# Performance work log

Measured on AMD Instinct MI355X. Metric: run time of the kernel, lower is better.

The kernel has to match this reference:

```python
import jax, jax.numpy as jnp
import numpy as np

MAXHD, MAXV, MINA, MAXA, DT = 100.0, 40.0, -4.0, 3.0, 0.1
NVEH, NT, H = 16384, 256, 20


def setup_inputs() -> dict:
    key = jax.random.key(0)
    ks = jax.random.split(key, 6)
    lead_speed = 10.0 + 5.0 * jax.random.normal(ks[0], (NVEH, NT), dtype=jnp.float32)
    lead_pos = 50.0 + 20.0 * jax.random.normal(ks[1], (NVEH, NT), dtype=jnp.float32)
    lead_inputs = jnp.stack([lead_pos, lead_speed], axis=2)  # (nveh, nt, 2)
    init_state = jnp.stack([
        5.0 * jax.random.normal(ks[2], (NVEH,), dtype=jnp.float32),
        10.0 + 2.0 * jax.random.normal(ks[3], (NVEH,), dtype=jnp.float32),
    ], axis=1)  # (nveh, 2) -> (pos, speed)
    return {
        "lead_inputs": lead_inputs,
        "init_state": init_state,
        "h0": jnp.zeros((NVEH, H), jnp.float32),
        "c0": jnp.zeros((NVEH, H), jnp.float32),
        "W": 0.3 * jax.random.normal(ks[4], (3, 4 * H), dtype=jnp.float32),
        "U": 0.2 * jax.random.normal(ks[5], (H, 4 * H), dtype=jnp.float32),
        "b": jnp.concatenate([jnp.zeros(H), jnp.ones(H), jnp.zeros(2 * H)]).astype(jnp.float32),  # unit forget bias
        "Wd": 0.3 * jax.random.normal(jax.random.fold_in(key, 7), (H, 1), dtype=jnp.float32),
        "bd": jnp.zeros((1,), jnp.float32),
    }


def reference(lead_inputs, init_state, h0, c0, W, U, b, Wd, bd):
    def step(carry, lead):
        pos, speed, h, c = carry
        curhd = (lead[:, 0] - pos) / MAXHD
        lead_v = lead[:, 1] / MAXV
        norm_v = speed / MAXV
        x = jnp.stack([curhd, norm_v, lead_v], axis=1)  # (nveh, 3)
        z = x @ W + h @ U + b  # (nveh, 4H), keras gate order i, f, g, o
        i, f, g, o = jnp.split(z, 4, axis=1)
        c = jax.nn.sigmoid(f) * c + jax.nn.sigmoid(i) * jnp.tanh(g)
        h = jax.nn.sigmoid(o) * jnp.tanh(c)
        out = (h @ Wd + bd)[:, 0]  # (nveh,)
        acc = (MAXA - MINA) * out + MINA
        speed = speed + DT * acc
        pos = pos + DT * acc  # faithful to source (uses acc, not speed)
        return (pos, speed, h, c), pos

    pos0, speed0 = init_state[:, 0], init_state[:, 1]
    (pos, speed, h, c), ys = jax.lax.scan(
        step, (pos0, speed0, h0, c0), jnp.swapaxes(lead_inputs, 0, 1))
    # tf.concat of nt (nveh,) tensors along -1 -> flat (nt*nveh,) in time-major order
    outputs = ys.reshape(-1)
    return outputs, speed, (h, c)
```

## Files before the change

### kernel.cpp

```cpp
#include <hip/hip_runtime.h>


#define NVEH 16384
#define NT   256
#define H    20

typedef float f32x4  __attribute__((ext_vector_type(4)));
typedef short bf16x8 __attribute__((ext_vector_type(8)));

#if __has_builtin(__builtin_amdgcn_exp2f)
#define EXP2(x) __builtin_amdgcn_exp2f(x)
#else
#define EXP2(x) __expf((x) * 0.69314718056f)
#endif
#define RCP(x) __builtin_amdgcn_rcpf(x)

__device__ __forceinline__ short f2bf(float f) {
    unsigned u = __builtin_bit_cast(unsigned, f);
    u += 0x7fffu + ((u >> 16) & 1u);
    return (short)(u >> 16);
}
__device__ __forceinline__ float bf2f(short s) {
    return __builtin_bit_cast(float, ((unsigned)(unsigned short)s) << 16);
}

__global__ __launch_bounds__(256, 1) void rnncf_kernel(
    const float* __restrict__ lead,
    const float* __restrict__ inits,
    const float* __restrict__ h0,
    const float* __restrict__ c0,
    const float* __restrict__ W,
    const float* __restrict__ U,
    const float* __restrict__ b,
    const float* __restrict__ Wd,
    const float* __restrict__ bd,
    float* __restrict__ out)
{
    __shared__ __attribute__((aligned(16))) short UT[96 * 32];

    const int tid  = threadIdx.x;
    const int lane = tid & 63;
    const int q    = lane >> 4;
    const int c    = lane & 15;
    const float L2E = 1.44269504f;
    const float N2L = -2.f * L2E;
    const float bdv = bd[0];
    const float biasK = 7.f * bdv - 4.f;

    for (int idx = tid; idx < 96 * 32; idx += 256) {
        int row = idx >> 5, k = idx & 31;
        int T = row >> 4, m = row & 15;
        int kq = k >> 3, ko = k & 7;
        float v = 0.f;
        if (T < 5) {
            int g = m & 3, j = 5 * (m >> 2) + T;
            int col = g * 20 + j;
            if      (ko < 5)             v = U[(5 * kq + ko) * 80 + col];
            else if (ko == 6 && kq < 3)  v = W[kq * 80 + col];
            else if (ko == 6)            v = b[col];
            v *= (g == 2) ? (2.f * L2E) : L2E;
        } else if ((m & 3) == 0) {
            if      (ko < 5)  v = 7.f * Wd[5 * kq + ko];
            else if (ko == 5) v = 1.f;
        }
        UT[idx] = f2bf(v);
    }

    const int veh = blockIdx.x * 64 + (tid >> 6) * 16 + c;

    float wcn[5][4], wd7[5], w7b[5];
#pragma unroll
    for (int T = 0; T < 5; ++T) {
        int j = 5 * q + T;
#pragma unroll
        for (int g = 0; g < 4; ++g) {
            int col = g * 20 + j;
            wcn[T][g] = -(-0.001f * W[col] + 0.0025f * W[80 + col])
                      * ((g == 2) ? (2.f * L2E) : L2E);
        }
        float w7 = 7.f * Wd[j];
        wd7[T] = w7;
        w7b[T] = bf2f(f2bf(w7));
    }

    bf16x8 Bf = {0, 0, 0, 0, 0, 0, 0, 0};
    float cst[5], hl[5];
    float rpart = 0.f, apart = 0.f;
#pragma unroll
    for (int T = 0; T < 5; ++T) {
        int j = 5 * q + T;
        float hv = h0[veh * H + j];
        cst[T] = c0[veh * H + j];
        hl[T] = hv;
        short hb = f2bf(hv);
        float hi = bf2f(hb);
        Bf[T] = hb;
        rpart = __builtin_fmaf(hv, wd7[T], rpart);
        rpart = __builtin_fmaf(-hi, w7b[T], rpart);
        apart = __builtin_fmaf(hv, wd7[T], apart);
    }
    Bf[5] = f2bf(rpart);
    apart += __shfl_xor(apart, 16);
    apart += __shfl_xor(apart, 32);

    float pos = inits[veh * 2 + 0];
    float spd = inits[veh * 2 + 1];
    {
        float a = apart + biasK;
        pos -= 0.1f * a;
        spd -= 0.1f * a;
    }

    const float2* lp0 = (const float2*)lead + (long)veh * NT;
    {
        float2 lu = lp0[0];
        float xv = (q == 0) ? (lu.x - pos) * 0.01f
                 : (q == 1) ? spd * 0.025f
                            : lu.y * 0.025f;
        if (q < 3) Bf[6] = f2bf(xv);
        else       Bf[6] = (short)0x3F80;
    }
    float2 lA = lp0[1];
    float2 lB = lp0[2];

    __syncthreads();

    bf16x8 A[6];
#pragma unroll
    for (int T = 0; T < 6; ++T)
        A[T] = *(const bf16x8*)&UT[(T * 16 + c) * 32 + q * 8];

    for (int t = 0; t < NT; ++t) {
        float2 lu = lA;
        lA = lB;
        int tn = t + 3; tn = (tn < NT) ? tn : NT - 1;
        lB = lp0[tn];

        f32x4 zero = {0.f, 0.f, 0.f, 0.f};
        f32x4 z[6];
#pragma unroll
        for (int T = 0; T < 6; ++T)
            z[T] = __builtin_amdgcn_mfma_f32_16x16x32_bf16(A[T], Bf, zero, 0, 0, 0);

        float acc = z[5][0] + biasK;
        pos = __builtin_fmaf(0.1f, acc, pos);
        spd = __builtin_fmaf(0.1f, acc, spd);
        if (q == 1 && t > 0)
            out[(size_t)(t - 1) * NVEH + veh] = pos;

        {
            float xv = (q == 0) ? (lu.x - pos) * 0.01f
                     : (q == 1) ? spd * 0.025f
                                : lu.y * 0.025f;
            if (q < 3) Bf[6] = f2bf(xv);
        }

        float rq = 0.f;
#pragma unroll
        for (int T = 0; T < 5; ++T) {
            float ei = EXP2(__builtin_fmaf(acc, wcn[T][0], -z[T][0]));
            float ef = EXP2(__builtin_fmaf(acc, wcn[T][1], -z[T][1]));
            float eg = EXP2(__builtin_fmaf(acc, wcn[T][2], -z[T][2]));
            float eo = EXP2(__builtin_fmaf(acc, wcn[T][3], -z[T][3]));
            float ii = RCP(1.f + ei);
            float ff = RCP(1.f + ef);
            float sg = RCP(1.f + eg);
            float oo = RCP(1.f + eo);
            float gg = __builtin_fmaf(2.f, sg, -1.f);
            float cc = __builtin_fmaf(ff, cst[T], ii * gg);
            cst[T] = cc;
            float ec = EXP2(N2L * cc);
            float st = RCP(1.f + ec);
            float hh = oo * __builtin_fmaf(2.f, st, -1.f);
            hl[T] = hh;
            unsigned u = __builtin_bit_cast(unsigned, hh);
            unsigned r = u + 0x7fffu + ((u >> 16) & 1u);
            Bf[T] = (short)(r >> 16);
            float hi = __builtin_bit_cast(float, r & 0xffff0000u);
            rq = __builtin_fmaf(hh, wd7[T], rq);
            rq = __builtin_fmaf(-hi, w7b[T], rq);
        }
        Bf[5] = f2bf(rq);
    }

    float ap = 0.f;
#pragma unroll
    for (int T = 0; T < 5; ++T) ap = __builtin_fmaf(hl[T], wd7[T], ap);
    ap += __shfl_xor(ap, 16);
    ap += __shfl_xor(ap, 32);
    float accF = ap + biasK;
    if (q == 1) out[(size_t)(NT - 1) * NVEH + veh] = pos + 0.1f * accF;
    if (q == 2) out[(size_t)NT * NVEH + veh]       = spd + 0.1f * accF;

    const int oH = NT * NVEH + NVEH;
    const int oC = oH + NVEH * H;
#pragma unroll
    for (int T = 0; T < 5; ++T) {
        int j = 5 * q + T;
        out[oH + veh * H + j] = hl[T];
        out[oC + veh * H + j] = cst[T];
    }
}

extern "C" void kernel_launch(void* const* d_in, const int* in_sizes, int n_in,
                              void* d_out, int out_size, void* d_ws, size_t ws_size,
                              hipStream_t stream) {
    const float* lead  = (const float*)d_in[0];
    const float* inits = (const float*)d_in[1];
    const float* h0    = (const float*)d_in[2];
    const float* c0    = (const float*)d_in[3];
    const float* W     = (const float*)d_in[4];
    const float* U     = (const float*)d_in[5];
    const float* b     = (const float*)d_in[6];
    const float* Wd    = (const float*)d_in[7];
    const float* bd    = (const float*)d_in[8];
    float* out = (float*)d_out;

    rnncf_kernel<<<NVEH / 64, 256, 0, stream>>>(lead, inits, h0, c0, W, U, b, Wd, bd, out);
}
```

Measured before the change: 213.8 us.

## Shorten LSTM recurrence critical path with merged reciprocals and packed bf16 conversion

The per-step gate math is reworked so that input and g-gate sigmoids share one reciprocal, as do the output gate and tanh(c). The cell state is kept prescaled by -2*log2(e) so it feeds exp2 directly. The h values are packed into the MFMA B operand with v_cvt_pk_bf16_f32 instead of manual rounding, and the residual dot product becomes a tree reduction. The scalar MFMA is issued first, and fused vector FMAs are used for the gate pre-activations. The goal is fewer transcendental and ALU ops on the serial time-step chain. In exchange, merging reciprocals risks overflow, which is clamped with fmin on the cell term, and the numerics change slightly.

```diff
diff --git a/kernel.cpp b/kernel.cpp
--- a/kernel.cpp
+++ b/kernel.cpp
@@ -6,7 +6,9 @@
 #define H    20
 
 typedef float f32x4  __attribute__((ext_vector_type(4)));
+typedef float f32x2  __attribute__((ext_vector_type(2)));
 typedef short bf16x8 __attribute__((ext_vector_type(8)));
+typedef unsigned u32x4 __attribute__((ext_vector_type(4)));
 
 #if __has_builtin(__builtin_amdgcn_exp2f)
 #define EXP2(x) __builtin_amdgcn_exp2f(x)
@@ -22,6 +24,11 @@
 }
 __device__ __forceinline__ float bf2f(short s) {
     return __builtin_bit_cast(float, ((unsigned)(unsigned short)s) << 16);
+}
+__device__ __forceinline__ unsigned cvtpk(float lo, float hi) {
+    unsigned r;
+    asm("v_cvt_pk_bf16_f32 %0, %1, %2" : "=v"(r) : "v"(lo), "v"(hi));
+    return r;
 }
 
 __global__ __launch_bounds__(256, 1) void rnncf_kernel(
@@ -44,6 +51,8 @@
     const int c    = lane & 15;
     const float L2E = 1.44269504f;
     const float N2L = -2.f * L2E;
+    const float P2L =  2.f * L2E;
+    const float IN2L = -0.34657359028f;
     const float bdv = bd[0];
     const float biasK = 7.f * bdv - 4.f;
 
@@ -68,38 +77,51 @@
 
     const int veh = blockIdx.x * 64 + (tid >> 6) * 16 + c;
 
-    float wcn[5][4], wd7[5], w7b[5];
+    f32x2 wif[5], wgo[5];
+    float wd7[5], w7b[5];
 #pragma unroll
     for (int T = 0; T < 5; ++T) {
         int j = 5 * q + T;
+        float wc[4];
 #pragma unroll
         for (int g = 0; g < 4; ++g) {
             int col = g * 20 + j;
-            wcn[T][g] = -(-0.001f * W[col] + 0.0025f * W[80 + col])
-                      * ((g == 2) ? (2.f * L2E) : L2E);
-        }
+            wc[g] = -(-0.001f * W[col] + 0.0025f * W[80 + col])
+                  * ((g == 2) ? (2.f * L2E) : L2E);
+        }
+        f32x2 a = {wc[0], wc[1]}; wif[T] = a;
+        f32x2 d = {wc[2], wc[3]}; wgo[T] = d;
         float w7 = 7.f * Wd[j];
         wd7[T] = w7;
         w7b[T] = bf2f(f2bf(w7));
     }
 
-    bf16x8 Bf = {0, 0, 0, 0, 0, 0, 0, 0};
-    float cst[5], hl[5];
+    u32x4 B;
+    float cst2[5], hl[5];
     float rpart = 0.f, apart = 0.f;
-#pragma unroll
-    for (int T = 0; T < 5; ++T) {
-        int j = 5 * q + T;
-        float hv = h0[veh * H + j];
-        cst[T] = c0[veh * H + j];
-        hl[T] = hv;
-        short hb = f2bf(hv);
-        float hi = bf2f(hb);
-        Bf[T] = hb;
-        rpart = __builtin_fmaf(hv, wd7[T], rpart);
-        rpart = __builtin_fmaf(-hi, w7b[T], rpart);
-        apart = __builtin_fmaf(hv, wd7[T], apart);
-    }
-    Bf[5] = f2bf(rpart);
+    {
+        unsigned w0 = 0, w1 = 0, w2 = 0;
+#pragma unroll
+        for (int T = 0; T < 5; ++T) {
+            int j = 5 * q + T;
+            float hv = h0[veh * H + j];
+            cst2[T] = N2L * c0[veh * H + j];
+            hl[T] = hv;
+            short hb = f2bf(hv);
+            float hi = bf2f(hb);
+            unsigned hs = (unsigned)(unsigned short)hb;
+            if      (T == 0) w0  = hs;
+            else if (T == 1) w0 |= hs << 16;
+            else if (T == 2) w1  = hs;
+            else if (T == 3) w1 |= hs << 16;
+            else             w2  = hs;
+            rpart = __builtin_fmaf(hv, wd7[T], rpart);
+            rpart = __builtin_fmaf(-hi, w7b[T], rpart);
+            apart = __builtin_fmaf(hv, wd7[T], apart);
+        }
+        w2 |= (unsigned)(unsigned short)f2bf(rpart) << 16;
+        B[0] = w0; B[1] = w1; B[2] = w2;
+    }
     apart += __shfl_xor(apart, 16);
     apart += __shfl_xor(apart, 32);
 
@@ -116,9 +138,9 @@
         float2 lu = lp0[0];
         float xv = (q == 0) ? (lu.x - pos) * 0.01f
                  : (q == 1) ? spd * 0.025f
-                            : lu.y * 0.025f;
-        if (q < 3) Bf[6] = f2bf(xv);
-        else       Bf[6] = (short)0x3F80;
+                 : (q == 2) ? lu.y * 0.025f
+                            : 1.0f;
+        B[3] = (unsigned)(unsigned short)f2bf(xv);
     }
     float2 lA = lp0[1];
     float2 lB = lp0[2];
@@ -137,50 +159,65 @@
         lB = lp0[tn];
 
         f32x4 zero = {0.f, 0.f, 0.f, 0.f};
-        f32x4 z[6];
-#pragma unroll
-        for (int T = 0; T < 6; ++T)
+        bf16x8 Bf = __builtin_bit_cast(bf16x8, B);
+        f32x4 z5 = __builtin_amdgcn_mfma_f32_16x16x32_bf16(A[5], Bf, zero, 0, 0, 0);
+        f32x4 z[5];
+#pragma unroll
+        for (int T = 0; T < 5; ++T)
             z[T] = __builtin_amdgcn_mfma_f32_16x16x32_bf16(A[T], Bf, zero, 0, 0, 0);
 
-        float acc = z[5][0] + biasK;
+        float acc = z5[0] + biasK;
         pos = __builtin_fmaf(0.1f, acc, pos);
         spd = __builtin_fmaf(0.1f, acc, spd);
         if (q == 1 && t > 0)
             out[(size_t)(t - 1) * NVEH + veh] = pos;
 
-        {
-            float xv = (q == 0) ? (lu.x - pos) * 0.01f
-                     : (q == 1) ? spd * 0.025f
-                                : lu.y * 0.025f;
-            if (q < 3) Bf[6] = f2bf(xv);
-        }
-
-        float rq = 0.f;
+        float xv = (q == 0) ? (lu.x - pos) * 0.01f
+                 : (q == 1) ? spd * 0.025f
+                 : (q == 2) ? lu.y * 0.025f
+                            : 1.0f;
+        unsigned d3 = cvtpk(xv, 0.f);
+
+        f32x2 acc2 = {acc, acc};
 #pragma unroll
         for (int T = 0; T < 5; ++T) {
-            float ei = EXP2(__builtin_fmaf(acc, wcn[T][0], -z[T][0]));
-            float ef = EXP2(__builtin_fmaf(acc, wcn[T][1], -z[T][1]));
-            float eg = EXP2(__builtin_fmaf(acc, wcn[T][2], -z[T][2]));
-            float eo = EXP2(__builtin_fmaf(acc, wcn[T][3], -z[T][3]));
-            float ii = RCP(1.f + ei);
-            float ff = RCP(1.f + ef);
-            float sg = RCP(1.f + eg);
-            float oo = RCP(1.f + eo);
-            float gg = __builtin_fmaf(2.f, sg, -1.f);
-            float cc = __builtin_fmaf(ff, cst[T], ii * gg);
-            cst[T] = cc;
-            float ec = EXP2(N2L * cc);
-            float st = RCP(1.f + ec);
-            float hh = oo * __builtin_fmaf(2.f, st, -1.f);
-            hl[T] = hh;
-            unsigned u = __builtin_bit_cast(unsigned, hh);
-            unsigned r = u + 0x7fffu + ((u >> 16) & 1u);
-            Bf[T] = (short)(r >> 16);
-            float hi = __builtin_bit_cast(float, r & 0xffff0000u);
-            rq = __builtin_fmaf(hh, wd7[T], rq);
-            rq = __builtin_fmaf(-hi, w7b[T], rq);
-        }
-        Bf[5] = f2bf(rq);
+            f32x2 zif = __builtin_shufflevector(z[T], z[T], 0, 1);
+            f32x2 zgo = __builtin_shufflevector(z[T], z[T], 2, 3);
+            f32x2 aif = __builtin_elementwise_fma(acc2, wif[T], -zif);
+            f32x2 ago = __builtin_elementwise_fma(acc2, wgo[T], -zgo);
+            float ei = EXP2(aif[0]);
+            float ef = EXP2(aif[1]);
+            float eg = EXP2(ago[0]);
+            float eo = EXP2(ago[1]);
+            float pi = 1.f + ei, pf = 1.f + ef, pg = 1.f + eg, po = 1.f + eo;
+            float Rig = RCP(pi * pg);
+            float ffv = RCP(pf);
+            float uu  = __builtin_fmaf(P2L, eg, N2L);
+            float t2  = uu * Rig;
+            float c2  = __builtin_fmaf(ffv, cst2[T], t2);
+            cst2[T] = c2;
+            float ec = EXP2(__builtin_fminf(c2, 80.f));
+            float pc = 1.f + ec;
+            float Roc = RCP(po * pc);
+            hl[T] = (1.f - ec) * Roc;
+        }
+
+        unsigned d0 = cvtpk(hl[0], hl[1]);
+        unsigned d1 = cvtpk(hl[2], hl[3]);
+        float hi0 = __builtin_bit_cast(float, d0 << 16);
+        float hi1 = __builtin_bit_cast(float, d0 & 0xffff0000u);
+        float hi2 = __builtin_bit_cast(float, d1 << 16);
+        float hi3 = __builtin_bit_cast(float, d1 & 0xffff0000u);
+        unsigned u4 = __builtin_bit_cast(unsigned, hl[4]);
+        float hi4 = __builtin_bit_cast(float, (u4 + 0x7fffu + ((u4 >> 16) & 1u)) & 0xffff0000u);
+        float r0 = __builtin_fmaf(hl[0], wd7[0], -(hi0 * w7b[0]));
+        float r1 = __builtin_fmaf(hl[1], wd7[1], -(hi1 * w7b[1]));
+        float r2 = __builtin_fmaf(hl[2], wd7[2], -(hi2 * w7b[2]));
+        float r3 = __builtin_fmaf(hl[3], wd7[3], -(hi3 * w7b[3]));
+        float r4 = __builtin_fmaf(hl[4], wd7[4], -(hi4 * w7b[4]));
+        float rq = ((r0 + r1) + (r2 + r3)) + r4;
+        unsigned d2 = cvtpk(hl[4], rq);
+        B[0] = d0; B[1] = d1; B[2] = d2; B[3] = d3;
     }
 
     float ap = 0.f;
@@ -198,7 +235,7 @@
     for (int T = 0; T < 5; ++T) {
         int j = 5 * q + T;
         out[oH + veh * H + j] = hl[T];
-        out[oC + veh * H + j] = cst[T];
+        out[oC + veh * H + j] = cst2[T] * IN2L;
     }
 }
 
```

Result: slower. 220.4 us (+3.1%).
